# Kernel optimization log

Measured on AMD Instinct MI355X. Metric: run time of the kernel, lower is better.

## Reference

```python
import jax, jax.numpy as jnp
import numpy as np

K, L = 9, 32


def conv1d(x, w):
    # x: [b, C, P], w: [O, C, 3]; padding=1 kernel=3 == SAME
    return jax.lax.conv_general_dilated(
        x, w, window_strides=(1,), padding='SAME',
        dimension_numbers=('NCH', 'OIH', 'NCH'))


def prior_surface(x, w1, w2, w3, w4):
    # x: [b, P]
    h = jax.nn.relu(conv1d(x[:, None, :], w1))
    h = jax.nn.relu(conv1d(h, w2))
    h = jax.nn.relu(conv1d(h, w3))
    out = x[:, None, :] + jax.nn.relu(conv1d(h, w4))
    return jnp.clip(out, 0.0, 1.0)[:, 0, :]


def setup_inputs() -> dict:
    key = jax.random.key(0)
    ks = jax.random.split(key, 9)
    b, E, M, P = 32, 20, 64, 3072
    d_split = 0.1 * jax.random.normal(ks[0], (b, E, M), jnp.float32)
    surf0 = jax.random.uniform(ks[1], (b, P), dtype=jnp.float32)
    clouds0 = jax.random.uniform(ks[2], (b, E, P), dtype=jnp.float32)
    # scale Phi so gradients stay in a sane range for the [0,1] clamps
    Phi_split = jax.random.normal(ks[3], (b, E, M, P), jnp.float32) / P
    rho_base = 0.1 * jax.random.uniform(ks[4], (b,), dtype=jnp.float32)
    rho = jnp.ones((K,), jnp.float32)

    def kaiming(k, shape):
        fan_in = shape[-2] * shape[-1]
        return jax.random.normal(k, shape, jnp.float32) * np.float32(np.sqrt(2.0 / fan_in))

    w1 = kaiming(ks[5], (K, L, 1, 3))
    w2 = kaiming(ks[6], (K, L, L, 3))
    w3 = kaiming(ks[7], (K, L, L, 3))
    w4 = kaiming(ks[8], (K, 1, L, 3))
    return {"d_split": d_split, "surf0": surf0, "clouds0": clouds0,
            "Phi_split": Phi_split, "rho_base": rho_base, "rho": rho,
            "w1": w1, "w2": w2, "w3": w3, "w4": w4, "n_epochs": 20}


def reference(d_split, surf0, clouds0, Phi_split, rho_base, rho, w1, w2, w3, w4, n_epochs):
    # d_split: [b,E,M], surf0: [b,P], clouds0: [b,E,P], Phi_split: [b,E,M,P], rho_base: [b]
    surf, clouds = surf0, clouds0
    out_surface, out_clouds = [], []
    for i in range(K):
        t0 = 1.0 - clouds                       # [b,E,P]
        t1 = t0 * t0
        tmp = clouds + t1 * surf[:, None, :]    # [b,E,P]
        y = jnp.einsum('bemp,bep->bem', Phi_split, tmp)          # Phi @ tmp
        t2 = jnp.einsum('bemp,bem->bep', Phi_split, y - d_split)  # PhiT @ resid
        # the torch loop over j accumulates grad_surf += 2*t2*t1; equivalent sum over E
        grad_surf = surf0 + 2.0 * jnp.sum(t2 * t1, axis=1)        # [b,P]
        grad_clouds = 2.0 * t2 - 4.0 * t2 * surf[:, None, :] * t0 # [b,E,P]
        rho_i = jnp.clip(rho[i], 0.1, 3.0)
        r_surf = surf - rho_base[:, None] * rho_i * grad_surf
        r_clouds = clouds - rho_base[:, None, None] * rho_i * grad_clouds
        surf = prior_surface(r_surf, w1[i], w2[i], w3[i], w4[i])
        clouds = jax.nn.relu(r_clouds)
        out_surface.append(surf)
        out_clouds.append(clouds)
    return (surf, clouds, jnp.stack(out_surface), jnp.stack(out_clouds))
```

## Files before the change

kernel.cpp:

```cpp
#include <hip/hip_runtime.h>

#define B_ 32
#define E_ 20
#define M_ 64
#define P_ 3072
#define K_ 9
#define BEP (B_ * E_ * P_)
#define TT2 192
#define NT2 16
#define BUFW 208

#define PHI_SCALE 65536.0f
#define PHI_INV   (1.0f / 65536.0f)

typedef float floatx2 __attribute__((ext_vector_type(2)));
typedef _Float16 half4v __attribute__((ext_vector_type(4)));

__device__ __forceinline__ unsigned int pack4_fp8(float f0, float f1, float f2, float f3)
{
    int w = 0;
    w = __builtin_amdgcn_cvt_pk_fp8_f32(f0, f1, w, false);
    w = __builtin_amdgcn_cvt_pk_fp8_f32(f2, f3, w, true);
    return (unsigned int)w;
}

template <int MODE>
__global__ __launch_bounds__(256) void k_A(
    const float* __restrict__ PhiF,
    const unsigned char* __restrict__ Phi8,
    unsigned char* __restrict__ Phi8w,
    const float* __restrict__ dsplit,
    const float* __restrict__ surf_cur,
    const float* __restrict__ clouds_cur,
    const float* __restrict__ rho_base,
    const float* __restrict__ rho_i,
    float* __restrict__ s2t1,
    float* __restrict__ out_clouds_i,
    float* __restrict__ out_clouds_final)
{
    __shared__ float s_tmp[P_];
    __shared__ float s_yr[M_];

    const int bid = blockIdx.x;
    const int b   = bid / E_;
    const int tid = threadIdx.x;
    const int wave = tid >> 6, lane = tid & 63;
    const size_t base = (size_t)bid * (M_ * P_);

    const float* ccur = clouds_cur + (size_t)bid * P_;
    const float* scur = surf_cur + (size_t)b * P_;

    {
        const float4* cl4 = reinterpret_cast<const float4*>(ccur);
        const float4* sf4 = reinterpret_cast<const float4*>(scur);
        for (int f = tid; f < P_ / 4; f += 256) {
            float4 c4 = cl4[f], s4 = sf4[f], tm;
            float t0x = 1.f - c4.x, t0y = 1.f - c4.y, t0z = 1.f - c4.z, t0w = 1.f - c4.w;
            tm.x = c4.x + t0x * t0x * s4.x;
            tm.y = c4.y + t0y * t0y * s4.y;
            tm.z = c4.z + t0z * t0z * s4.z;
            tm.w = c4.w + t0w * t0w * s4.w;
            reinterpret_cast<float4*>(s_tmp)[f] = tm;
        }
    }
    __syncthreads();

    if constexpr (MODE == 0) {
        #pragma unroll 2
        for (int r = 0; r < 16; ++r) {
            const int mg = (wave << 4) + r;
            const float4* prow = reinterpret_cast<const float4*>(PhiF + base + (size_t)mg * P_);
            unsigned int* orow = reinterpret_cast<unsigned int*>(Phi8w + base + (size_t)mg * P_);
            float acc = 0.f;
            #pragma unroll
            for (int j = 0; j < 12; ++j) {
                const int f = j * 64 + lane;
                float4 v = prow[f];
                float4 t = reinterpret_cast<const float4*>(s_tmp)[f];
                acc += v.x * t.x + v.y * t.y + v.z * t.z + v.w * t.w;
                orow[f] = pack4_fp8(v.x * PHI_SCALE, v.y * PHI_SCALE,
                                    v.z * PHI_SCALE, v.w * PHI_SCALE);
            }
            #pragma unroll
            for (int off = 32; off > 0; off >>= 1)
                acc += __shfl_down(acc, off, 64);
            if (lane == 0)
                s_yr[mg] = acc - dsplit[bid * M_ + mg];
        }
    } else {
        #pragma unroll 2
        for (int r = 0; r < 16; ++r) {
            const int mg = (wave << 4) + r;
            const uint2* prow = reinterpret_cast<const uint2*>(Phi8 + base + (size_t)mg * P_);
            float acc = 0.f;
            #pragma unroll
            for (int j = 0; j < 6; ++j) {
                const int f = j * 64 + lane;
                uint2 w = prow[f];
                floatx2 l0 = __builtin_amdgcn_cvt_pk_f32_fp8((int)w.x, false);
                floatx2 h0 = __builtin_amdgcn_cvt_pk_f32_fp8((int)w.x, true);
                floatx2 l1 = __builtin_amdgcn_cvt_pk_f32_fp8((int)w.y, false);
                floatx2 h1 = __builtin_amdgcn_cvt_pk_f32_fp8((int)w.y, true);
                const float4 a  = reinterpret_cast<const float4*>(s_tmp)[2 * f];
                const float4 bb = reinterpret_cast<const float4*>(s_tmp)[2 * f + 1];
                acc += l0.x * a.x + l0.y * a.y + h0.x * a.z + h0.y * a.w
                     + l1.x * bb.x + l1.y * bb.y + h1.x * bb.z + h1.y * bb.w;
            }
            #pragma unroll
            for (int off = 32; off > 0; off >>= 1)
                acc += __shfl_down(acc, off, 64);
            if (lane == 0)
                s_yr[mg] = acc * PHI_INV - dsplit[bid * M_ + mg];
        }
    }
    __syncthreads();

    {
        const unsigned char* p8 = ((MODE == 0) ? Phi8w : Phi8) + base + tid * 12;
        float acc[12];
        #pragma unroll
        for (int k = 0; k < 12; ++k) acc[k] = 0.f;
        #pragma unroll 4
        for (int m = 0; m < M_; ++m) {
            const float ym = s_yr[m];
            uint3 w = *reinterpret_cast<const uint3*>(p8 + (size_t)m * P_);
            floatx2 c0 = __builtin_amdgcn_cvt_pk_f32_fp8((int)w.x, false);
            floatx2 c1 = __builtin_amdgcn_cvt_pk_f32_fp8((int)w.x, true);
            floatx2 c2 = __builtin_amdgcn_cvt_pk_f32_fp8((int)w.y, false);
            floatx2 c3 = __builtin_amdgcn_cvt_pk_f32_fp8((int)w.y, true);
            floatx2 c4 = __builtin_amdgcn_cvt_pk_f32_fp8((int)w.z, false);
            floatx2 c5 = __builtin_amdgcn_cvt_pk_f32_fp8((int)w.z, true);
            acc[0] += c0.x * ym; acc[1]  += c0.y * ym;
            acc[2] += c1.x * ym; acc[3]  += c1.y * ym;
            acc[4] += c2.x * ym; acc[5]  += c2.y * ym;
            acc[6] += c3.x * ym; acc[7]  += c3.y * ym;
            acc[8] += c4.x * ym; acc[9]  += c4.y * ym;
            acc[10]+= c5.x * ym; acc[11] += c5.y * ym;
        }

        const float s = rho_base[b] * fminf(fmaxf(*rho_i, 0.1f), 3.0f);
        const int p0t = tid * 12;
        const size_t gi = (size_t)bid * P_ + p0t;
        #pragma unroll
        for (int k4 = 0; k4 < 3; ++k4) {
            float4 cv = *reinterpret_cast<const float4*>(ccur + p0t + k4 * 4);
            float4 sv = *reinterpret_cast<const float4*>(scur + p0t + k4 * 4);
            float4 stv, ncv;
#define EPI(C, KK)                                                      \
            {                                                           \
                float t2v = acc[k4 * 4 + KK] * PHI_INV;                 \
                float t0  = 1.f - cv.C;                                 \
                stv.C = t2v * t0 * t0;                                  \
                float gc = 2.f * t2v * (1.f - 2.f * sv.C * t0);         \
                ncv.C = fmaxf(cv.C - s * gc, 0.f);                      \
            }
            EPI(x, 0) EPI(y, 1) EPI(z, 2) EPI(w, 3)
#undef EPI
            *reinterpret_cast<float4*>(s2t1 + gi + k4 * 4) = stv;
            *reinterpret_cast<float4*>(out_clouds_i + gi + k4 * 4) = ncv;
            if (out_clouds_final)
                *reinterpret_cast<float4*>(out_clouds_final + gi + k4 * 4) = ncv;
        }
    }
}

__global__ __launch_bounds__(256) void k_surf(
    const float* __restrict__ surf0,
    const float* __restrict__ surf_cur,
    const float* __restrict__ s2t1,
    const float* __restrict__ rho_base,
    const float* __restrict__ rho_i,
    const float* __restrict__ w1,
    const float* __restrict__ w2,
    const float* __restrict__ w3,
    const float* __restrict__ w4,
    float* __restrict__ out_surface_i,
    float* __restrict__ out_surf_final)
{
    __shared__ float sx[BUFW];
    __shared__ float bufA[32 * BUFW];
    __shared__ float bufB[32 * BUFW];
    __shared__ _Float16 sw2h[32 * 32 * 4];
    __shared__ _Float16 sw3h[32 * 32 * 4];
    __shared__ float sw1s[32 * 4];
    __shared__ float sw4s[32 * 4];

    const int tid = threadIdx.x;
    const int b  = blockIdx.x >> 4;
    const int p0 = (blockIdx.x & 15) * TT2;
    const size_t bP = (size_t)b * P_;

    for (int idx = tid; idx < 1024; idx += 256) {
        const int c = idx >> 5, o = idx & 31;
        const int src = (o * 32 + c) * 3;
        sw2h[idx * 4 + 0] = (_Float16)w2[src + 0];
        sw2h[idx * 4 + 1] = (_Float16)w2[src + 1];
        sw2h[idx * 4 + 2] = (_Float16)w2[src + 2];
        sw2h[idx * 4 + 3] = (_Float16)0.f;
        sw3h[idx * 4 + 0] = (_Float16)w3[src + 0];
        sw3h[idx * 4 + 1] = (_Float16)w3[src + 1];
        sw3h[idx * 4 + 2] = (_Float16)w3[src + 2];
        sw3h[idx * 4 + 3] = (_Float16)0.f;
    }
    if (tid < 32) {
        sw1s[tid * 4 + 0] = w1[tid * 3 + 0];
        sw1s[tid * 4 + 1] = w1[tid * 3 + 1];
        sw1s[tid * 4 + 2] = w1[tid * 3 + 2];
        sw1s[tid * 4 + 3] = 0.f;
        sw4s[tid * 4 + 0] = w4[tid * 3 + 0];
        sw4s[tid * 4 + 1] = w4[tid * 3 + 1];
        sw4s[tid * 4 + 2] = w4[tid * 3 + 2];
        sw4s[tid * 4 + 3] = 0.f;
    }

    const float s = rho_base[b] * fminf(fmaxf(*rho_i, 0.1f), 3.0f);

    for (int j = tid; j < BUFW; j += 256) {
        float v = 0.f;
        const int p = p0 + j - 4;
        if (j < TT2 + 8 && p >= 0 && p < P_) {
            float g = surf0[bP + p];
            #pragma unroll
            for (int e = 0; e < E_; ++e)
                g += 2.f * s2t1[((size_t)(b * E_ + e)) * P_ + p];
            v = surf_cur[bP + p] - s * g;
        }
        sx[j] = v;
    }
    __syncthreads();

    {
        const int Wout = TT2 + 6;
        const int QG = 50;
        const int pstart = p0 - 3;
        for (int g = tid; g < 32 * QG; g += 256) {
            const int o = g / QG, q = g - o * QG, j0 = q << 2;
            const float4 i03 = *reinterpret_cast<const float4*>(&sx[j0]);
            const float2 i45 = *reinterpret_cast<const float2*>(&sx[j0 + 4]);
            const float4 wv = *reinterpret_cast<const float4*>(&sw1s[o * 4]);
            float a0 = i03.x * wv.x + i03.y * wv.y + i03.z * wv.z;
            float a1 = i03.y * wv.x + i03.z * wv.y + i03.w * wv.z;
            float a2 = i03.z * wv.x + i03.w * wv.y + i45.x * wv.z;
            float a3 = i03.w * wv.x + i45.x * wv.y + i45.y * wv.z;
            float* op = &bufA[o * BUFW + j0];
            const int p = pstart + j0;
            if (j0     < Wout) op[0] = (p     >= 0 && p     < P_) ? fmaxf(a0, 0.f) : 0.f;
            if (j0 + 1 < Wout) op[1] = (p + 1 >= 0 && p + 1 < P_) ? fmaxf(a1, 0.f) : 0.f;
            if (j0 + 2 < Wout) op[2] = (p + 2 >= 0 && p + 2 < P_) ? fmaxf(a2, 0.f) : 0.f;
            if (j0 + 3 < Wout) op[3] = (p + 3 >= 0 && p + 3 < P_) ? fmaxf(a3, 0.f) : 0.f;
        }
    }
    __syncthreads();

    for (int layer = 0; layer < 2; ++layer) {
        const float* inb  = layer ? bufB : bufA;
        float* outb       = layer ? bufA : bufB;
        const _Float16* w = layer ? sw3h : sw2h;
        const int Wout    = layer ? (TT2 + 2) : (TT2 + 4);
        const int pstart  = layer ? (p0 - 1) : (p0 - 2);
        const int QG = (Wout + 3) >> 2;
        for (int g = tid; g < 8 * QG; g += 256) {
            const int oo = g / QG, q = g - oo * QG, j0 = q << 2;
            float a[4][4];
            #pragma unroll
            for (int ol = 0; ol < 4; ++ol)
                a[ol][0] = a[ol][1] = a[ol][2] = a[ol][3] = 0.f;
            #pragma unroll 4
            for (int c = 0; c < 32; ++c) {
                const float* ip = inb + c * BUFW + j0;
                const float4 i03 = *reinterpret_cast<const float4*>(ip);
                const float2 i45 = *reinterpret_cast<const float2*>(ip + 4);
                const float f0 = i03.x, f1 = i03.y, f2 = i03.z,
                            f3 = i03.w, f4 = i45.x, f5 = i45.y;
                const _Float16* wb = w + (c * 32 + oo * 4) * 4;
                #pragma unroll
                for (int ol = 0; ol < 4; ++ol) {
                    half4v wv = *reinterpret_cast<const half4v*>(wb + ol * 4);
                    const float w0 = wv[0], w1v = wv[1], w2v = wv[2];
                    a[ol][0] += f0 * w0 + f1 * w1v + f2 * w2v;
                    a[ol][1] += f1 * w0 + f2 * w1v + f3 * w2v;
                    a[ol][2] += f2 * w0 + f3 * w1v + f4 * w2v;
                    a[ol][3] += f3 * w0 + f4 * w1v + f5 * w2v;
                }
            }
            const int p = pstart + j0;
            #pragma unroll
            for (int ol = 0; ol < 4; ++ol) {
                float* op = outb + (oo * 4 + ol) * BUFW + j0;
                if (j0     < Wout) op[0] = (p     >= 0 && p     < P_) ? fmaxf(a[ol][0], 0.f) : 0.f;
                if (j0 + 1 < Wout) op[1] = (p + 1 >= 0 && p + 1 < P_) ? fmaxf(a[ol][1], 0.f) : 0.f;
                if (j0 + 2 < Wout) op[2] = (p + 2 >= 0 && p + 2 < P_) ? fmaxf(a[ol][2], 0.f) : 0.f;
                if (j0 + 3 < Wout) op[3] = (p + 3 >= 0 && p + 3 < P_) ? fmaxf(a[ol][3], 0.f) : 0.f;
            }
        }
        __syncthreads();
    }

    {
        float* orow = out_surface_i + bP + p0;
        for (int g = tid; g < TT2 / 2; g += 256) {
            const int j0 = g * 2;
            float a0 = 0.f, a1 = 0.f;
            #pragma unroll 8
            for (int c = 0; c < 32; ++c) {
                const float* ip = &bufA[c * BUFW + j0];
                const float2 iA = *reinterpret_cast<const float2*>(ip);
                const float2 iB = *reinterpret_cast<const float2*>(ip + 2);
                const float4 wv = *reinterpret_cast<const float4*>(&sw4s[c * 4]);
                a0 += iA.x * wv.x + iA.y * wv.y + iB.x * wv.z;
                a1 += iA.y * wv.x + iB.x * wv.y + iB.y * wv.z;
            }
            const float x0 = sx[j0 + 4], x1 = sx[j0 + 5];
            float2 ov;
            ov.x = fminf(fmaxf(x0 + fmaxf(a0, 0.f), 0.f), 1.f);
            ov.y = fminf(fmaxf(x1 + fmaxf(a1, 0.f), 0.f), 1.f);
            *reinterpret_cast<float2*>(orow + j0) = ov;
            if (out_surf_final)
                *reinterpret_cast<float2*>(out_surf_final + bP + p0 + j0) = ov;
        }
    }
}

extern "C" void kernel_launch(void* const* d_in, const int* in_sizes, int n_in,
                              void* d_out, int out_size, void* d_ws, size_t ws_size,
                              hipStream_t stream)
{
    (void)in_sizes; (void)n_in; (void)out_size; (void)ws_size;

    const float* dsplit   = (const float*)d_in[0];
    const float* surf0    = (const float*)d_in[1];
    const float* clouds0  = (const float*)d_in[2];
    const float* Phi      = (const float*)d_in[3];
    const float* rho_base = (const float*)d_in[4];
    const float* rho      = (const float*)d_in[5];
    const float* w1       = (const float*)d_in[6];
    const float* w2       = (const float*)d_in[7];
    const float* w3       = (const float*)d_in[8];
    const float* w4       = (const float*)d_in[9];

    float* out = (float*)d_out;
    float* out_surf_final   = out;
    float* out_clouds_final = out + (size_t)B_ * P_;
    float* out_surface      = out_clouds_final + (size_t)BEP;
    float* out_clouds       = out_surface + (size_t)K_ * B_ * P_;

    unsigned char* phi8 = (unsigned char*)d_ws;
    float* s2t1 = (float*)((unsigned char*)d_ws + (size_t)B_ * E_ * M_ * P_);

    for (int i = 0; i < K_; ++i) {
        const float* scur = (i == 0) ? surf0   : out_surface + (size_t)(i - 1) * B_ * P_;
        const float* ccur = (i == 0) ? clouds0 : out_clouds + (size_t)(i - 1) * BEP;
        float* oc_i = out_clouds + (size_t)i * BEP;
        float* ocF  = (i == K_ - 1) ? out_clouds_final : nullptr;
        float* osF  = (i == K_ - 1) ? out_surf_final : nullptr;

        if (i == 0)
            k_A<0><<<dim3(B_ * E_), dim3(256), 0, stream>>>(
                Phi, nullptr, phi8, dsplit, scur, ccur,
                rho_base, rho + i, s2t1, oc_i, ocF);
        else
            k_A<1><<<dim3(B_ * E_), dim3(256), 0, stream>>>(
                nullptr, phi8, nullptr, dsplit, scur, ccur,
                rho_base, rho + i, s2t1, oc_i, ocF);

        k_surf<<<dim3(B_ * NT2), dim3(256), 0, stream>>>(
            surf0, scur, s2t1, rho_base, rho + i,
            w1 + (size_t)i * 96, w2 + (size_t)i * 3072,
            w3 + (size_t)i * 3072, w4 + (size_t)i * 96,
            out_surface + (size_t)i * B_ * P_, osF);
    }
}
```

Baseline: 904.6 us.

## Double k_A block size and split M reduction across two thread halves

Grows each k_A block to 512 threads. The first pass now gives each wave 8 Phi rows and reads them with 16-byte fp8 loads. The transpose pass splits the 64 M rows between two 256-thread halves and combines their partial sums through a new shared buffer before the epilogue. The aim is more memory parallelism per block on this bandwidth-bound pass. In exchange it adds 12 KB of shared memory, an extra barrier, and idle threads in the epilogue, and larger blocks may lower occupancy. An unused DOT8 macro is left in the code.

After: 925.4 us. +2.3%, slower.

```diff
diff --git a/kernel.cpp b/kernel.cpp
--- a/kernel.cpp
+++ b/kernel.cpp
@@ -25,7 +25,7 @@
 }
 
 template <int MODE>
-__global__ __launch_bounds__(256) void k_A(
+__global__ __launch_bounds__(512) void k_A(
     const float* __restrict__ PhiF,
     const unsigned char* __restrict__ Phi8,
     unsigned char* __restrict__ Phi8w,
@@ -39,6 +39,7 @@
     float* __restrict__ out_clouds_final)
 {
     __shared__ float s_tmp[P_];
+    __shared__ float s_part[P_];
     __shared__ float s_yr[M_];
 
     const int bid = blockIdx.x;
@@ -53,7 +54,7 @@
     {
         const float4* cl4 = reinterpret_cast<const float4*>(ccur);
         const float4* sf4 = reinterpret_cast<const float4*>(scur);
-        for (int f = tid; f < P_ / 4; f += 256) {
+        for (int f = tid; f < P_ / 4; f += 512) {
             float4 c4 = cl4[f], s4 = sf4[f], tm;
             float t0x = 1.f - c4.x, t0y = 1.f - c4.y, t0z = 1.f - c4.z, t0w = 1.f - c4.w;
             tm.x = c4.x + t0x * t0x * s4.x;
@@ -67,8 +68,8 @@
 
     if constexpr (MODE == 0) {
         #pragma unroll 2
-        for (int r = 0; r < 16; ++r) {
-            const int mg = (wave << 4) + r;
+        for (int r = 0; r < 8; ++r) {
+            const int mg = (wave << 3) + r;
             const float4* prow = reinterpret_cast<const float4*>(PhiF + base + (size_t)mg * P_);
             unsigned int* orow = reinterpret_cast<unsigned int*>(Phi8w + base + (size_t)mg * P_);
             float acc = 0.f;
@@ -89,22 +90,39 @@
         }
     } else {
         #pragma unroll 2
-        for (int r = 0; r < 16; ++r) {
-            const int mg = (wave << 4) + r;
-            const uint2* prow = reinterpret_cast<const uint2*>(Phi8 + base + (size_t)mg * P_);
+        for (int r = 0; r < 8; ++r) {
+            const int mg = (wave << 3) + r;
+            const uint4* prow = reinterpret_cast<const uint4*>(Phi8 + base + (size_t)mg * P_);
             float acc = 0.f;
             #pragma unroll
-            for (int j = 0; j < 6; ++j) {
+            for (int j = 0; j < 3; ++j) {
                 const int f = j * 64 + lane;
-                uint2 w = prow[f];
-                floatx2 l0 = __builtin_amdgcn_cvt_pk_f32_fp8((int)w.x, false);
-                floatx2 h0 = __builtin_amdgcn_cvt_pk_f32_fp8((int)w.x, true);
-                floatx2 l1 = __builtin_amdgcn_cvt_pk_f32_fp8((int)w.y, false);
-                floatx2 h1 = __builtin_amdgcn_cvt_pk_f32_fp8((int)w.y, true);
-                const float4 a  = reinterpret_cast<const float4*>(s_tmp)[2 * f];
-                const float4 bb = reinterpret_cast<const float4*>(s_tmp)[2 * f + 1];
-                acc += l0.x * a.x + l0.y * a.y + h0.x * a.z + h0.y * a.w
-                     + l1.x * bb.x + l1.y * bb.y + h1.x * bb.z + h1.y * bb.w;
+                uint4 w = prow[f];
+                const float4* t4 = reinterpret_cast<const float4*>(s_tmp) + 4 * f;
+#define DOT8(W, T0, T1)                                                   \
+                {                                                         \
+                    floatx2 lo = __builtin_amdgcn_cvt_pk_f32_fp8((int)(W), false); \
+                    floatx2 hi = __builtin_amdgcn_cvt_pk_f32_fp8((int)(W), true);  \
+                    const float4 ta = (T0), tb = (T1);                    \
+                    acc += lo.x * ta.x + lo.y * ta.y + hi.x * ta.z + hi.y * ta.w;  \
+                    (void)tb;                                             \
+                }
+                {
+                    floatx2 l0 = __builtin_amdgcn_cvt_pk_f32_fp8((int)w.x, false);
+                    floatx2 h0 = __builtin_amdgcn_cvt_pk_f32_fp8((int)w.x, true);
+                    floatx2 l1 = __builtin_amdgcn_cvt_pk_f32_fp8((int)w.y, false);
+                    floatx2 h1 = __builtin_amdgcn_cvt_pk_f32_fp8((int)w.y, true);
+                    floatx2 l2 = __builtin_amdgcn_cvt_pk_f32_fp8((int)w.z, false);
+                    floatx2 h2 = __builtin_amdgcn_cvt_pk_f32_fp8((int)w.z, true);
+                    floatx2 l3 = __builtin_amdgcn_cvt_pk_f32_fp8((int)w.w, false);
+                    floatx2 h3 = __builtin_amdgcn_cvt_pk_f32_fp8((int)w.w, true);
+                    const float4 t0 = t4[0], t1 = t4[1], t2 = t4[2], t3 = t4[3];
+                    acc += l0.x * t0.x + l0.y * t0.y + h0.x * t0.z + h0.y * t0.w
+                         + l1.x * t1.x + l1.y * t1.y + h1.x * t1.z + h1.y * t1.w
+                         + l2.x * t2.x + l2.y * t2.y + h2.x * t2.z + h2.y * t2.w
+                         + l3.x * t3.x + l3.y * t3.y + h3.x * t3.z + h3.y * t3.w;
+                }
+#undef DOT8
             }
             #pragma unroll
             for (int off = 32; off > 0; off >>= 1)
@@ -115,14 +133,18 @@
     }
     __syncthreads();
 
+    const int half = tid >> 8;
+    const int t    = tid & 255;
+    const int p0t  = t * 12;
     {
-        const unsigned char* p8 = ((MODE == 0) ? Phi8w : Phi8) + base + tid * 12;
+        const unsigned char* p8 = ((MODE == 0) ? Phi8w : Phi8)
+                                  + base + (size_t)(half * 32) * P_ + p0t;
         float acc[12];
         #pragma unroll
         for (int k = 0; k < 12; ++k) acc[k] = 0.f;
         #pragma unroll 4
-        for (int m = 0; m < M_; ++m) {
-            const float ym = s_yr[m];
+        for (int m = 0; m < 32; ++m) {
+            const float ym = s_yr[half * 32 + m];
             uint3 w = *reinterpret_cast<const uint3*>(p8 + (size_t)m * P_);
             floatx2 c0 = __builtin_amdgcn_cvt_pk_f32_fp8((int)w.x, false);
             floatx2 c1 = __builtin_amdgcn_cvt_pk_f32_fp8((int)w.x, true);
@@ -138,28 +160,47 @@
             acc[10]+= c5.x * ym; acc[11] += c5.y * ym;
         }
 
-        const float s = rho_base[b] * fminf(fmaxf(*rho_i, 0.1f), 3.0f);
-        const int p0t = tid * 12;
-        const size_t gi = (size_t)bid * P_ + p0t;
-        #pragma unroll
-        for (int k4 = 0; k4 < 3; ++k4) {
-            float4 cv = *reinterpret_cast<const float4*>(ccur + p0t + k4 * 4);
-            float4 sv = *reinterpret_cast<const float4*>(scur + p0t + k4 * 4);
-            float4 stv, ncv;
+        if (half == 1) {
+            #pragma unroll
+            for (int k4 = 0; k4 < 3; ++k4)
+                reinterpret_cast<float4*>(s_part)[t * 3 + k4] =
+                    make_float4(acc[k4 * 4], acc[k4 * 4 + 1],
+                                acc[k4 * 4 + 2], acc[k4 * 4 + 3]);
+        }
+        __syncthreads();
+
+        if (half == 0) {
+            #pragma unroll
+            for (int k4 = 0; k4 < 3; ++k4) {
+                float4 pp = reinterpret_cast<const float4*>(s_part)[t * 3 + k4];
+                acc[k4 * 4 + 0] += pp.x;
+                acc[k4 * 4 + 1] += pp.y;
+                acc[k4 * 4 + 2] += pp.z;
+                acc[k4 * 4 + 3] += pp.w;
+            }
+
+            const float s = rho_base[b] * fminf(fmaxf(*rho_i, 0.1f), 3.0f);
+            const size_t gi = (size_t)bid * P_ + p0t;
+            #pragma unroll
+            for (int k4 = 0; k4 < 3; ++k4) {
+                float4 cv = *reinterpret_cast<const float4*>(ccur + p0t + k4 * 4);
+                float4 sv = *reinterpret_cast<const float4*>(scur + p0t + k4 * 4);
+                float4 stv, ncv;
 #define EPI(C, KK)                                                      \
-            {                                                           \
-                float t2v = acc[k4 * 4 + KK] * PHI_INV;                 \
-                float t0  = 1.f - cv.C;                                 \
-                stv.C = t2v * t0 * t0;                                  \
-                float gc = 2.f * t2v * (1.f - 2.f * sv.C * t0);         \
-                ncv.C = fmaxf(cv.C - s * gc, 0.f);                      \
-            }
-            EPI(x, 0) EPI(y, 1) EPI(z, 2) EPI(w, 3)
+                {                                                       \
+                    float t2v = acc[k4 * 4 + KK] * PHI_INV;             \
+                    float t0  = 1.f - cv.C;                             \
+                    stv.C = t2v * t0 * t0;                              \
+                    float gc = 2.f * t2v * (1.f - 2.f * sv.C * t0);     \
+                    ncv.C = fmaxf(cv.C - s * gc, 0.f);                  \
+                }
+                EPI(x, 0) EPI(y, 1) EPI(z, 2) EPI(w, 3)
 #undef EPI
-            *reinterpret_cast<float4*>(s2t1 + gi + k4 * 4) = stv;
-            *reinterpret_cast<float4*>(out_clouds_i + gi + k4 * 4) = ncv;
-            if (out_clouds_final)
-                *reinterpret_cast<float4*>(out_clouds_final + gi + k4 * 4) = ncv;
+                *reinterpret_cast<float4*>(s2t1 + gi + k4 * 4) = stv;
+                *reinterpret_cast<float4*>(out_clouds_i + gi + k4 * 4) = ncv;
+                if (out_clouds_final)
+                    *reinterpret_cast<float4*>(out_clouds_final + gi + k4 * 4) = ncv;
+            }
         }
     }
 }
@@ -355,11 +396,11 @@
         float* osF  = (i == K_ - 1) ? out_surf_final : nullptr;
 
         if (i == 0)
-            k_A<0><<<dim3(B_ * E_), dim3(256), 0, stream>>>(
+            k_A<0><<<dim3(B_ * E_), dim3(512), 0, stream>>>(
                 Phi, nullptr, phi8, dsplit, scur, ccur,
                 rho_base, rho + i, s2t1, oc_i, ocF);
         else
-            k_A<1><<<dim3(B_ * E_), dim3(256), 0, stream>>>(
+            k_A<1><<<dim3(B_ * E_), dim3(512), 0, stream>>>(
                 nullptr, phi8, nullptr, dsplit, scur, ccur,
                 rho_base, rho + i, s2t1, oc_i, ocF);
 
```
